# Optimization experiments

Hardware: AMD Instinct MI355X
Metric: run time of the kernel (lower is better)

The kernel has to match this reference:

```python
import jax, jax.numpy as jnp
import numpy as np

LEVEL = 3
NDIM = 2 ** LEVEL  # 8 quantized dims
SCALE = 0.9990000128746033


def setup_inputs() -> dict:
    key = jax.random.key(0)
    k1, k2, k3 = jax.random.split(key, 3)
    B, T, D = 8, 8192, 1280
    x = jax.random.normal(k1, (B, T, D), dtype=jnp.float32)
    # nn.Linear(D, 8): weight (8, D), bias (8)
    W = jax.random.normal(k2, (NDIM, D), dtype=jnp.float32) / np.sqrt(D)
    b = jax.random.normal(k3, (NDIM,), dtype=jnp.float32) * 0.01
    return {"x": x, "W": W, "b": b}


def reference(x, W, b):
    B, T, D = x.shape
    xf = x.reshape(-1, D)                       # (B*T, D)
    h = jnp.einsum('nd,kd->nk', xf, W) + b      # (B*T, 8) skinny GEMM
    h = jnp.tanh(h.astype(jnp.float32)) * SCALE
    h = jnp.round(h) + 1.0                      # ternary {0,1,2}
    powers = jnp.power(jnp.float32(LEVEL), jnp.arange(NDIM, dtype=jnp.float32))
    mu = jnp.sum(h * powers, axis=-1)           # base-3 index as float
    return mu.reshape(B, T).astype(jnp.int32)
```

## Files before the change

kernel.cpp:

```cpp
#include <hip/hip_runtime.h>
#include <math.h>

#define DIM 1280
#define NDIM 8
#define CHUNKS 5

__global__ __launch_bounds__(256, 2)
void fsq_kernel(const float* __restrict__ x, const float* __restrict__ W,
                const float* __restrict__ b, int* __restrict__ out, int n_tok) {
    const int lane    = threadIdx.x & 63;
    const int wave    = (int)((blockIdx.x * blockDim.x + threadIdx.x) >> 6);
    const int n_waves = (int)((gridDim.x * blockDim.x) >> 6);

    const float T = (float)atanh(0.5 / 0.9990000128746033);

    float4 w[CHUNKS][NDIM];
    #pragma unroll
    for (int c = 0; c < CHUNKS; ++c) {
        #pragma unroll
        for (int k = 0; k < NDIM; ++k) {
            w[c][k] = *(const float4*)(W + k * DIM + c * 256 + lane * 4);
        }
    }

    float bias[NDIM];
    #pragma unroll
    for (int k = 0; k < NDIM; ++k) bias[k] = b[k];

    for (int t = wave; t < n_tok; t += n_waves) {
        const float4* xp = (const float4*)(x + (size_t)t * DIM);
        float4 xv[CHUNKS];
        #pragma unroll
        for (int c = 0; c < CHUNKS; ++c) xv[c] = xp[c * 64 + lane];

        float acc[NDIM];
        #pragma unroll
        for (int k = 0; k < NDIM; ++k) acc[k] = 0.0f;

        #pragma unroll
        for (int c = 0; c < CHUNKS; ++c) {
            #pragma unroll
            for (int k = 0; k < NDIM; ++k) {
                acc[k] = fmaf(xv[c].x, w[c][k].x, acc[k]);
                acc[k] = fmaf(xv[c].y, w[c][k].y, acc[k]);
                acc[k] = fmaf(xv[c].z, w[c][k].z, acc[k]);
                acc[k] = fmaf(xv[c].w, w[c][k].w, acc[k]);
            }
        }

        #pragma unroll
        for (int k = 0; k < NDIM; ++k) {
            #pragma unroll
            for (int off = 32; off >= 1; off >>= 1) {
                acc[k] += __shfl_xor(acc[k], off, 64);
            }
        }

        int mu = 0, p3 = 1;
        #pragma unroll
        for (int k = 0; k < NDIM; ++k) {
            float h = acc[k] + bias[k];
            int d = 1 + (h > T ? 1 : 0) - (h < -T ? 1 : 0);
            mu += d * p3;
            p3 *= 3;
        }
        if (lane == 0) out[t] = mu;
    }
}

extern "C" void kernel_launch(void* const* d_in, const int* in_sizes, int n_in,
                              void* d_out, int out_size, void* d_ws, size_t ws_size,
                              hipStream_t stream) {
    const float* x = (const float*)d_in[0];
    const float* W = (const float*)d_in[1];
    const float* b = (const float*)d_in[2];
    int* out = (int*)d_out;

    const int n_tok = in_sizes[0] / DIM;
    const int blocks = 2048;
    fsq_kernel<<<blocks, 256, 0, stream>>>(x, W, b, out, n_tok);
}
```

Before: 436.7 us.

## Prefetch next token into registers and use butterfly transpose-reduce across lanes

Loads the next token's x row into registers while the current dot products and reductions run, so load latency overlaps compute. Replaces eight independent full-wave shuffle reductions with a butterfly reduce-scatter that leaves each 8-lane group holding one output dimension, then combines the base-3 digits with three shuffles. Halves the grid so each wave handles more tokens. This raises register pressure from holding the prefetched rows alongside the current accumulators.

```diff
diff --git a/kernel.cpp b/kernel.cpp
--- a/kernel.cpp
+++ b/kernel.cpp
@@ -23,16 +23,23 @@
         }
     }
 
-    float bias[NDIM];
-    #pragma unroll
-    for (int k = 0; k < NDIM; ++k) bias[k] = b[k];
+    const int b5 = (lane >> 5) & 1;
+    const int b4 = (lane >> 4) & 1;
+    const int b3 = (lane >> 3) & 1;
+    const int kk = 4 * b5 + 2 * b4 + b3;
+    const float bk  = b[kk];
+    const int   p3k = (kk & 1 ? 3 : 1) * (kk & 2 ? 9 : 1) * (kk & 4 ? 81 : 1);
+
+    if (wave >= n_tok) return;
+
+    float4 xv[CHUNKS];
+    {
+        const float4* xp = (const float4*)(x + (size_t)wave * DIM);
+        #pragma unroll
+        for (int c = 0; c < CHUNKS; ++c) xv[c] = xp[c * 64 + lane];
+    }
 
     for (int t = wave; t < n_tok; t += n_waves) {
-        const float4* xp = (const float4*)(x + (size_t)t * DIM);
-        float4 xv[CHUNKS];
-        #pragma unroll
-        for (int c = 0; c < CHUNKS; ++c) xv[c] = xp[c * 64 + lane];
-
         float acc[NDIM];
         #pragma unroll
         for (int k = 0; k < NDIM; ++k) acc[k] = 0.0f;
@@ -48,22 +55,43 @@
             }
         }
 
-        #pragma unroll
-        for (int k = 0; k < NDIM; ++k) {
+        const int tn = t + n_waves;
+        if (tn < n_tok) {
+            const float4* xp = (const float4*)(x + (size_t)tn * DIM);
             #pragma unroll
-            for (int off = 32; off >= 1; off >>= 1) {
-                acc[k] += __shfl_xor(acc[k], off, 64);
-            }
+            for (int c = 0; c < CHUNKS; ++c) xv[c] = xp[c * 64 + lane];
         }
 
-        int mu = 0, p3 = 1;
+        float r4[4];
         #pragma unroll
-        for (int k = 0; k < NDIM; ++k) {
-            float h = acc[k] + bias[k];
-            int d = 1 + (h > T ? 1 : 0) - (h < -T ? 1 : 0);
-            mu += d * p3;
-            p3 *= 3;
+        for (int i = 0; i < 4; ++i) {
+            float keep = b5 ? acc[i + 4] : acc[i];
+            float send = b5 ? acc[i]     : acc[i + 4];
+            r4[i] = keep + __shfl_xor(send, 32, 64);
         }
+        float r2[2];
+        #pragma unroll
+        for (int j = 0; j < 2; ++j) {
+            float keep = b4 ? r4[j + 2] : r4[j];
+            float send = b4 ? r4[j]     : r4[j + 2];
+            r2[j] = keep + __shfl_xor(send, 16, 64);
+        }
+        float s;
+        {
+            float keep = b3 ? r2[1] : r2[0];
+            float send = b3 ? r2[0] : r2[1];
+            s = keep + __shfl_xor(send, 8, 64);
+        }
+        s += __shfl_xor(s, 4, 64);
+        s += __shfl_xor(s, 2, 64);
+        s += __shfl_xor(s, 1, 64);
+
+        const float h = s + bk;
+        const int   d = 1 + (h > T ? 1 : 0) - (h < -T ? 1 : 0);
+        int mu = d * p3k;
+        mu += __shfl_xor(mu, 32, 64);
+        mu += __shfl_xor(mu, 16, 64);
+        mu += __shfl_xor(mu, 8, 64);
         if (lane == 0) out[t] = mu;
     }
 }
@@ -77,6 +105,6 @@
     int* out = (int*)d_out;
 
     const int n_tok = in_sizes[0] / DIM;
-    const int blocks = 2048;
+    const int blocks = 1024;
     fsq_kernel<<<blocks, 256, 0, stream>>>(x, W, b, out, n_tok);
 }
```

After: 439.5 us. Within noise of the previous version (+0.7%).
